# Optimization experiments

Measured on AMD Instinct MI355X. Metric: run time of the kernel, lower is better.

## Reference

```python
import jax, jax.numpy as jnp
import numpy as np

DELTA = 0.5  # EMA coefficient from __init__
B, N, CAT, FEAT, K = 8, 32768, 128, 128, 64


def setup_inputs() -> dict:
    key = jax.random.key(0)
    k1, k2 = jax.random.split(key)
    inp = jax.random.normal(k1, (B, N, CAT), dtype=jnp.float32)
    # nn.init.constant(weight, 1/sqrt(in_features))
    weight = jnp.full((CAT, FEAT), 1.0 / np.sqrt(FEAT), dtype=jnp.float32)
    keys = jnp.arange(K, dtype=jnp.int32)  # unique feat_dict keys, in [0, category)
    values = jax.random.normal(k2, (K, FEAT), dtype=jnp.float32)
    return {"input": inp, "weight": weight, "keys": keys, "values": values}


def reference(input, weight, keys, values):
    # output = (input @ weight).permute(0, 2, 1): (B, N, CAT) x (CAT, FEAT) -> (B, FEAT, N)
    output = jnp.einsum('bnc,cf->bfn', input, weight)
    # Per-key EMA update followed by scalar-L2-norm row overwrite (faithful to
    # torch: weight[key] = ||delta*w_k + (1-delta)*v_k||_2 broadcast over the row).
    new_rows = DELTA * weight[keys] + (1.0 - DELTA) * values           # (K, FEAT)
    norms = jnp.sqrt(jnp.sum(new_rows * new_rows, axis=1, keepdims=True))  # (K, 1)
    new_weight = weight.at[keys].set(jnp.broadcast_to(norms, new_rows.shape))
    return output, new_weight
```

## Files before the change

kernel.cpp:

```cpp
#include <hip/hip_runtime.h>
#include <math.h>

constexpr int B_ = 8, N_ = 32768, CAT_ = 128, FEAT_ = 128, K_ = 64;
constexpr float DELTA_ = 0.5f;

typedef __bf16 bf16x8 __attribute__((ext_vector_type(8)));
typedef float f32x4 __attribute__((ext_vector_type(4)));
typedef float f32x16 __attribute__((ext_vector_type(16)));

constexpr int BLOCK = 512;
constexpr int NPB   = 256;
constexpr int GEMM_BLOCKS = (B_ * N_) / NPB;

__global__ void prep_kernel(const float* __restrict__ weight,
                            const int* __restrict__ keys,
                            const float* __restrict__ values,
                            float* __restrict__ outw,
                            __bf16* __restrict__ wTs)
{
    const int r = blockIdx.x;
    const int t = threadIdx.x;
    float w = weight[r * FEAT_ + t];
    wTs[t * CAT_ + (r ^ ((t & 7) << 3))] = (__bf16)w;

    bool keyed = false;
    for (int i = 0; i < K_; ++i) keyed |= (keys[i] == r);
    if (!keyed) outw[r * FEAT_ + t] = w;

    if (r < K_ && t < 64) {
        const int key = keys[r];
        float a0 = DELTA_ * weight[key * FEAT_ + t]      + (1.0f - DELTA_) * values[r * FEAT_ + t];
        float a1 = DELTA_ * weight[key * FEAT_ + t + 64] + (1.0f - DELTA_) * values[r * FEAT_ + t + 64];
        float ss = a0 * a0 + a1 * a1;
        #pragma unroll
        for (int off = 32; off > 0; off >>= 1)
            ss += __shfl_down(ss, off, 64);
        float nrm = sqrtf(__shfl(ss, 0, 64));
        outw[key * FEAT_ + t]      = nrm;
        outw[key * FEAT_ + t + 64] = nrm;
    }
}

__global__ __launch_bounds__(BLOCK, 2) void gemm_kernel(
    const float* __restrict__ input,
    const __bf16* __restrict__ wTs,
    float* __restrict__ out)
{
    __shared__ __bf16 wt[FEAT_ * CAT_];

    const int tid  = threadIdx.x;
    const int wid  = tid >> 6;
    const int lane = tid & 63;

    #pragma unroll
    for (int j = 0; j < 4; ++j) {
        int off = j * 8192 + wid * 1024;
        __builtin_amdgcn_global_load_lds(
            (const __attribute__((address_space(1))) void*)((const char*)wTs + off + lane * 16),
            (__attribute__((address_space(3))) void*)((char*)wt + off),
            16, 0, 0);
    }

    const int nl = lane & 31;
    const int kg = lane >> 5;
    const int bid = blockIdx.x;
    const int b   = bid >> 7;
    const int nb  = bid & 127;
    const int n0  = nb * NPB + wid * 32;

    f32x16 acc[4];
    #pragma unroll
    for (int i = 0; i < 4; ++i)
        acc[i] = (f32x16)0.0f;

    const float* inp = input + ((size_t)b * N_ + n0 + nl) * CAT_;

    __syncthreads();

    #pragma unroll
    for (int ck = 0; ck < 8; ++ck) {
        const int c0 = ck * 16 + kg * 8;
        f32x4 v0 = *(const f32x4*)(inp + c0);
        f32x4 v1 = *(const f32x4*)(inp + c0 + 4);
        bf16x8 bfrag;
        #pragma unroll
        for (int e = 0; e < 4; ++e) {
            bfrag[e]     = (__bf16)v0[e];
            bfrag[e + 4] = (__bf16)v1[e];
        }
        #pragma unroll
        for (int mt = 0; mt < 4; ++mt) {
            const int f = mt * 32 + nl;
            bf16x8 af = *(const bf16x8*)&wt[f * CAT_ + (c0 ^ ((f & 7) << 3))];
            acc[mt] = __builtin_amdgcn_mfma_f32_32x32x16_bf16(af, bfrag, acc[mt], 0, 0, 0);
        }
    }

    float* outp = out + (size_t)b * FEAT_ * N_ + n0 + nl;
    #pragma unroll
    for (int mt = 0; mt < 4; ++mt) {
        #pragma unroll
        for (int r = 0; r < 16; ++r) {
            const int f = mt * 32 + (r & 3) + 8 * (r >> 2) + 4 * kg;
            __builtin_nontemporal_store(acc[mt][r], outp + (size_t)f * N_);
        }
    }
}

constexpr int LDSTR = 136;
constexpr int FB_BLOCKS = (B_ * N_) / 128;

__global__ __launch_bounds__(256, 4) void ocm_fused(
    const float* __restrict__ input,
    const float* __restrict__ weight,
    const int* __restrict__ keys,
    const float* __restrict__ values,
    float* __restrict__ out)
{
    const int bid = blockIdx.x;
    const int tid = threadIdx.x;

    if (bid >= FB_BLOCKS) {
        float* outw = out + (size_t)B_ * FEAT_ * N_;
        const int r = bid - FB_BLOCKS;
        bool keyed = false;
        for (int i = 0; i < K_; ++i) keyed |= (keys[i] == r);
        if (!keyed && tid < FEAT_)
            outw[r * FEAT_ + tid] = weight[r * FEAT_ + tid];
        if (r < K_ && tid < 64) {
            const int key = keys[r];
            float a0 = DELTA_ * weight[key * FEAT_ + tid]      + (1.0f - DELTA_) * values[r * FEAT_ + tid];
            float a1 = DELTA_ * weight[key * FEAT_ + tid + 64] + (1.0f - DELTA_) * values[r * FEAT_ + tid + 64];
            float ss = a0 * a0 + a1 * a1;
            #pragma unroll
            for (int off = 32; off > 0; off >>= 1)
                ss += __shfl_down(ss, off, 64);
            float nrm = sqrtf(__shfl(ss, 0, 64));
            outw[key * FEAT_ + tid]      = nrm;
            outw[key * FEAT_ + tid + 64] = nrm;
        }
        return;
    }

    __shared__ __bf16 wt[FEAT_ * LDSTR];
    #pragma unroll
    for (int j = 0; j < (CAT_ * FEAT_) / 256; ++j) {
        int i = tid + j * 256;
        int c = i >> 7;
        int f = i & (FEAT_ - 1);
        wt[f * LDSTR + c] = (__bf16)weight[i];
    }
    __syncthreads();

    const int wid  = tid >> 6;
    const int lane = tid & 63;
    const int qlo  = lane & 15;
    const int qhi  = lane >> 4;
    const int b    = bid >> 8;
    const int nb   = bid & 255;
    const int n0   = nb * 128 + wid * 32;

    f32x4 acc[8][2];
    #pragma unroll
    for (int i = 0; i < 8; ++i)
        #pragma unroll
        for (int j = 0; j < 2; ++j)
            acc[i][j] = (f32x4)0.0f;

    const float* in_base = input + ((size_t)b * N_ + n0) * CAT_;

    #pragma unroll
    for (int ck = 0; ck < 4; ++ck) {
        bf16x8 bfrag[2];
        #pragma unroll
        for (int nt = 0; nt < 2; ++nt) {
            const float* p = in_base + (size_t)(nt * 16 + qlo) * CAT_ + ck * 32 + qhi * 8;
            f32x4 v0 = *(const f32x4*)p;
            f32x4 v1 = *(const f32x4*)(p + 4);
            bf16x8 t;
            t[0] = (__bf16)v0[0]; t[1] = (__bf16)v0[1]; t[2] = (__bf16)v0[2]; t[3] = (__bf16)v0[3];
            t[4] = (__bf16)v1[0]; t[5] = (__bf16)v1[1]; t[6] = (__bf16)v1[2]; t[7] = (__bf16)v1[3];
            bfrag[nt] = t;
        }
        #pragma unroll
        for (int mt = 0; mt < 8; ++mt) {
            bf16x8 afrag = *(const bf16x8*)&wt[(mt * 16 + qlo) * LDSTR + ck * 32 + qhi * 8];
            acc[mt][0] = __builtin_amdgcn_mfma_f32_16x16x32_bf16(afrag, bfrag[0], acc[mt][0], 0, 0, 0);
            acc[mt][1] = __builtin_amdgcn_mfma_f32_16x16x32_bf16(afrag, bfrag[1], acc[mt][1], 0, 0, 0);
        }
    }

    float* outp = out + (size_t)b * FEAT_ * N_ + n0;
    #pragma unroll
    for (int mt = 0; mt < 8; ++mt) {
        #pragma unroll
        for (int nt = 0; nt < 2; ++nt) {
            #pragma unroll
            for (int r = 0; r < 4; ++r) {
                int f = mt * 16 + qhi * 4 + r;
                outp[(size_t)f * N_ + nt * 16 + qlo] = acc[mt][nt][r];
            }
        }
    }
}

extern "C" void kernel_launch(void* const* d_in, const int* in_sizes, int n_in,
                              void* d_out, int out_size, void* d_ws, size_t ws_size,
                              hipStream_t stream) {
    const float* input  = (const float*)d_in[0];
    const float* weight = (const float*)d_in[1];
    const int*   keys   = (const int*)d_in[2];
    const float* values = (const float*)d_in[3];
    float* out = (float*)d_out;

    if (ws_size >= (size_t)CAT_ * FEAT_ * sizeof(__bf16)) {
        __bf16* wTs = (__bf16*)d_ws;
        float* outw = out + (size_t)B_ * FEAT_ * N_;
        prep_kernel<<<CAT_, FEAT_, 0, stream>>>(weight, keys, values, outw, wTs);
        gemm_kernel<<<GEMM_BLOCKS, BLOCK, 0, stream>>>(input, wTs, out);
    } else {
        ocm_fused<<<FB_BLOCKS + CAT_, 256, 0, stream>>>(input, weight, keys, values, out);
    }
}
```

Measured before the change: 51.87 us.

## Double-buffer input slabs into LDS via async global-to-LDS loads

The GEMM kernel now stages each 16-column slab of the input tile into a double-buffered LDS region with global_load_lds, prefetching the next slab while computing on the current one. Previously each lane issued direct global vector loads per k-chunk. The aim is to overlap input fetch latency with MFMA work, at the cost of 32 KB extra LDS per block (which may lower occupancy) and a __syncthreads per k-step.

```diff
diff --git a/kernel.cpp b/kernel.cpp
--- a/kernel.cpp
+++ b/kernel.cpp
@@ -11,6 +11,9 @@
 constexpr int BLOCK = 512;
 constexpr int NPB   = 256;
 constexpr int GEMM_BLOCKS = (B_ * N_) / NPB;
+
+#define AS1 __attribute__((address_space(1)))
+#define AS3 __attribute__((address_space(3)))
 
 __global__ void prep_kernel(const float* __restrict__ weight,
                             const int* __restrict__ keys,
@@ -47,56 +50,81 @@
     float* __restrict__ out)
 {
     __shared__ __bf16 wt[FEAT_ * CAT_];
+    __shared__ float  islab[2 * 4096];
 
     const int tid  = threadIdx.x;
     const int wid  = tid >> 6;
     const int lane = tid & 63;
 
+    const int bid = blockIdx.x;
+    const int b   = bid >> 7;
+    const int nb  = bid & 127;
+    const int nbase = nb * NPB;
+    const size_t rowbase = (size_t)b * N_ + nbase;
+
     #pragma unroll
     for (int j = 0; j < 4; ++j) {
         int off = j * 8192 + wid * 1024;
         __builtin_amdgcn_global_load_lds(
-            (const __attribute__((address_space(1))) void*)((const char*)wTs + off + lane * 16),
-            (__attribute__((address_space(3))) void*)((char*)wt + off),
-            16, 0, 0);
-    }
+            (const AS1 void*)((const char*)wTs + off + lane * 16),
+            (AS3 void*)((char*)wt + off), 16, 0, 0);
+    }
+
+    #define STAGE_SLAB(s, dbuf)                                               \
+        {                                                                     \
+            _Pragma("unroll")                                                 \
+            for (int i = 0; i < 2; ++i) {                                     \
+                const int L  = i * 8192 + tid * 16;                           \
+                const int c4 = L >> 12;                                       \
+                const int r  = (L >> 4) & 255;                                \
+                const float* src = input + (rowbase + r) * CAT_ + (s) * 16 + c4 * 4; \
+                __builtin_amdgcn_global_load_lds(                             \
+                    (const AS1 void*)src,                                     \
+                    (AS3 void*)((char*)islab + (dbuf) * 16384 + i * 8192 + wid * 1024), \
+                    16, 0, 0);                                                \
+            }                                                                 \
+        }
+
+    STAGE_SLAB(0, 0);
 
     const int nl = lane & 31;
     const int kg = lane >> 5;
-    const int bid = blockIdx.x;
-    const int b   = bid >> 7;
-    const int nb  = bid & 127;
-    const int n0  = nb * NPB + wid * 32;
+    const int rloc = wid * 32 + nl;
 
     f32x16 acc[4];
     #pragma unroll
     for (int i = 0; i < 4; ++i)
         acc[i] = (f32x16)0.0f;
 
-    const float* inp = input + ((size_t)b * N_ + n0 + nl) * CAT_;
-
     __syncthreads();
 
     #pragma unroll
     for (int ck = 0; ck < 8; ++ck) {
-        const int c0 = ck * 16 + kg * 8;
-        f32x4 v0 = *(const f32x4*)(inp + c0);
-        f32x4 v1 = *(const f32x4*)(inp + c0 + 4);
+        const int buf = ck & 1;
+        if (ck < 7) STAGE_SLAB(ck + 1, buf ^ 1);
+
+        const char* sb = (const char*)islab + buf * 16384;
+        f32x4 v0 = *(const f32x4*)(sb + (2 * kg) * 4096 + rloc * 16);
+        f32x4 v1 = *(const f32x4*)(sb + (2 * kg + 1) * 4096 + rloc * 16);
         bf16x8 bfrag;
         #pragma unroll
         for (int e = 0; e < 4; ++e) {
             bfrag[e]     = (__bf16)v0[e];
             bfrag[e + 4] = (__bf16)v1[e];
         }
+
+        const int c0 = ck * 16 + kg * 8;
         #pragma unroll
         for (int mt = 0; mt < 4; ++mt) {
             const int f = mt * 32 + nl;
             bf16x8 af = *(const bf16x8*)&wt[f * CAT_ + (c0 ^ ((f & 7) << 3))];
             acc[mt] = __builtin_amdgcn_mfma_f32_32x32x16_bf16(af, bfrag, acc[mt], 0, 0, 0);
         }
-    }
-
-    float* outp = out + (size_t)b * FEAT_ * N_ + n0 + nl;
+
+        __syncthreads();
+    }
+
+    float* outp = out + (size_t)b * FEAT_ * N_ + nbase + wid * 32 + nl;
     #pragma unroll
     for (int mt = 0; mt < 4; ++mt) {
         #pragma unroll
@@ -105,6 +133,7 @@
             __builtin_nontemporal_store(acc[mt][r], outp + (size_t)f * N_);
         }
     }
+    #undef STAGE_SLAB
 }
 
 constexpr int LDSTR = 136;
```

Result: slower. 55.45 us (+6.9%).
